# Performance work log

Hardware: AMD Instinct MI355X
Metric: run time of the kernel (lower is better)

Reference implementation:

```python
import jax, jax.numpy as jnp
import numpy as np
from jax import lax

DN = ('NCHW', 'OIHW', 'NCHW')


def setup_inputs() -> dict:
    key = jax.random.key(0)
    ks = jax.random.split(key, 7)
    B, IC, OC, H, W = 8, 64, 64, 128, 128
    return {
        'x': jax.random.normal(ks[0], (B, IC, H, W), jnp.float32),
        'w3': jax.random.normal(ks[1], (OC, IC, 3, 3), jnp.float32) * 0.05,
        'b3': jax.random.normal(ks[2], (OC,), jnp.float32) * 0.05,
        'w5': jax.random.normal(ks[3], (OC, IC, 5, 5), jnp.float32) * 0.05,
        'b5': jax.random.normal(ks[4], (OC,), jnp.float32) * 0.05,
        'wr': jax.random.normal(ks[5], (OC, 10, 1, 1), jnp.float32) * 0.1,
        'br': jax.random.normal(ks[6], (OC,), jnp.float32) * 0.05,
    }


def reference(x, w3, b3, w5, b5, wr, br):
    # Two 'same' convs (k=3 pad 1, k=5 pad 2) as in layers['5']
    y3 = lax.conv_general_dilated(x, w3, (1, 1), 'SAME', dimension_numbers=DN) + b3[None, :, None, None]
    y5 = lax.conv_general_dilated(x, w5, (1, 1), 'SAME', dimension_numbers=DN) + b5[None, :, None, None]
    B, C, H, W = y3.shape
    # The nested pad/crop loop == 9 zero-padded unit shifts of y3:
    # stackedFeatures order per channel: [y5, shift(sh=0,sw=0..2), shift(sh=1,...), ...]
    # shifted[h, w] = y3[h + 1 - sw, w + 1 - sh] with zero padding.
    P = jnp.pad(y3, ((0, 0), (0, 0), (1, 1), (1, 1)))
    shifts = [P[:, :, 2 - sw:2 - sw + H, 2 - sh:2 - sh + W]
              for sh in range(3) for sw in range(3)]
    stacked = jnp.stack([y5] + shifts, axis=2)  # [B, C, 10, H, W]
    # remap: grouped 1x1 conv, groups=OC, 10 in-channels per group
    out = jnp.einsum('bcghw,cg->bchw', stacked, wr[:, :, 0, 0]) + br[None, :, None, None]
    return out
```

## Files before the change

kernel.cpp:

```cpp
#include <hip/hip_runtime.h>

typedef unsigned short u16;
typedef unsigned int u32;
typedef __attribute__((ext_vector_type(8))) short short8;
typedef __attribute__((ext_vector_type(4))) short short4v;
typedef __attribute__((ext_vector_type(4))) float floatx4;

#define HH 128
#define WW 128
#define ICN 64
#define OCN 64
#define XP 72

__device__ __forceinline__ float bf2f(u16 u) {
    u32 b = ((u32)u) << 16;
    return __builtin_bit_cast(float, b);
}
__device__ __forceinline__ u16 f2bf(float f) {
    u32 b = __builtin_bit_cast(u32, f);
    b += 0x7FFFu + ((b >> 16) & 1u);
    return (u16)(b >> 16);
}

#define W3P_BYTE 256
#define W5P_BYTE 74240
#define SCAL_BYTE 279296
#define XT_BYTE 282624
#define Y3T_BYTE 17059840
#define N_W3P 36864
#define N_W5P 102400
#define N_SCAL 832
#define PACK_N (N_W3P + N_W5P + N_SCAL)

__global__ __launch_bounds__(256) void sniff_kernel(const u16* __restrict__ xu,
                                                    int* __restrict__ flag) {
    __shared__ int cnt;
    if (threadIdx.x == 0) cnt = 0;
    __syncthreads();
    int c = 0;
    for (int k = 0; k < 8; ++k) {
        int idx = 2 * (threadIdx.x * 8 + k);
        u16 u = xu[idx];
        int e = (u >> 7) & 0xFF;
        if (e >= 140) c++;
    }
    atomicAdd(&cnt, c);
    __syncthreads();
    if (threadIdx.x == 0) *flag = (cnt >= 8) ? 1 : 0;
}

__device__ __forceinline__ float load_any(const void* p, int i, int isf32) {
    return isf32 ? ((const float*)p)[i] : bf2f(((const u16*)p)[i]);
}

__global__ __launch_bounds__(256) void prepack(
        const void* w3, const void* b3, const void* w5, const void* b5,
        const void* wr, const void* br, const int* __restrict__ flag,
        u16* __restrict__ w3p, u16* __restrict__ w5p, float* __restrict__ scal) {
    int i = blockIdx.x * 256 + threadIdx.x;
    if (i >= PACK_N) return;
    int f = *flag;
    if (i < N_W3P + N_W5P) {
        int is5 = (i >= N_W3P);
        int ii = is5 ? i - N_W3P : i;
        int j = ii & 7, lane = (ii >> 3) & 63, mt = (ii >> 9) & 3, ks = ii >> 11;
        int oc = mt * 16 + (lane & 15);
        int k = ks * 32 + ((lane >> 4) & 3) * 8 + j;
        int tap = k >> 6, ic = k & 63;
        float v;
        if (is5) v = load_any(w5, (oc * 64 + ic) * 25 + tap, f);
        else     v = load_any(w3, (oc * 64 + ic) * 9 + tap, f);
        u16 o = f2bf(v);
        if (is5) w5p[ii] = o; else w3p[ii] = o;
    } else {
        int i2 = i - N_W3P - N_W5P;
        float v;
        if (i2 < 64)       v = load_any(b3, i2, f);
        else if (i2 < 128) v = load_any(b5, i2 - 64, f);
        else if (i2 < 768) v = load_any(wr, i2 - 128, f);
        else               v = load_any(br, i2 - 768, f);
        scal[i2] = v;
    }
}

__global__ __launch_bounds__(256) void transpose_x(
        const void* __restrict__ x, const int* __restrict__ flag,
        u16* __restrict__ xt) {
    __shared__ u16 tbuf[32 * XP];
    const int b = blockIdx.z, h = blockIdx.y, w0 = blockIdx.x * 32;
    const int t = threadIdx.x;
    const int f = *flag;
    if (f) {
        const int w2 = t & 15, ic = t >> 4;
#pragma unroll
        for (int p = 0; p < 4; ++p) {
            int icc = ic + p * 16;
            const float* src = (const float*)x +
                (((size_t)(b * 64 + icc) * 128 + h) * 128 + w0 + 2 * w2);
            float2 v = *(const float2*)src;
            tbuf[(2 * w2) * XP + icc]     = f2bf(v.x);
            tbuf[(2 * w2 + 1) * XP + icc] = f2bf(v.y);
        }
    } else {
        const int w4 = t & 7, ic = t >> 3;
#pragma unroll
        for (int p = 0; p < 2; ++p) {
            int icc = ic + p * 32;
            const u16* src = (const u16*)x +
                (((size_t)(b * 64 + icc) * 128 + h) * 128 + w0 + 4 * w4);
            short4v v = *(const short4v*)src;
#pragma unroll
            for (int e = 0; e < 4; ++e)
                tbuf[(4 * w4 + e) * XP + icc] = (u16)v[e];
        }
    }
    __syncthreads();
    const int w = t >> 3, q = t & 7;
    short8 v = *(const short8*)&tbuf[w * XP + q * 8];
    *(short8*)(xt + ((size_t)((b * 128 + h) * 128) + w0 + w) * 64 + q * 8) = v;
}

__device__ __forceinline__ void stage_tile(
        const u16* __restrict__ src, u16* __restrict__ dst,
        int b, int h0, int w0, int halo, int cols, int npx, int iters, int tid) {
    const int q8 = tid & 7, p0 = tid >> 3;
    for (int it = 0; it < iters; ++it) {
        int px = p0 + it * 32;
        if (px < npx) {
            int r = px / cols, c = px - r * cols;
            int gh = h0 + r - halo, gw = w0 + c - halo;
            short8 v = {0, 0, 0, 0, 0, 0, 0, 0};
            if ((unsigned)gh < (unsigned)HH && (unsigned)gw < (unsigned)WW)
                v = *(const short8*)(src +
                        ((size_t)((b * 128 + gh) * 128 + gw)) * 64 + q8 * 8);
            *(short8*)&dst[px * XP + q8 * 8] = v;
        }
    }
}

#define LOAD_A(dst, wp, ks)                                                    \
    {                                                                          \
        const u16* _ap = (wp) + (size_t)(ks) * 2048 + lane * 8;                \
        _Pragma("unroll") for (int _s = 0; _s < 2; ++_s)                       \
            _Pragma("unroll") for (int _mt = 0; _mt < 4; ++_mt)                \
                dst[_s][_mt] = *(const short8*)(_ap + _s * 2048 + _mt * 512);  \
    }

#define DO_TAP(afr, kh, kw, COLS)                                              \
    {                                                                          \
        short8 bb[2][4];                                                       \
        int rbase = (wv4 + (kh)) * (COLS) + cb + (kw);                         \
        _Pragma("unroll") for (int nt = 0; nt < 4; ++nt)                       \
            _Pragma("unroll") for (int s = 0; s < 2; ++s)                      \
                bb[s][nt] = *(const short8*)&xs[(rbase + nt * (COLS)) * XP +   \
                                                s * 32 + q * 8];               \
        _Pragma("unroll") for (int s = 0; s < 2; ++s)                          \
            _Pragma("unroll") for (int nt = 0; nt < 4; ++nt)                   \
                _Pragma("unroll") for (int mt = 0; mt < 4; ++mt)               \
                    acc[mt][nt] = __builtin_amdgcn_mfma_f32_16x16x32_bf16(     \
                        afr[s][mt], bb[s][nt], acc[mt][nt], 0, 0, 0);          \
    }

__global__ __launch_bounds__(256, 2) void conv3_mfma(
        const u16* __restrict__ xt, const u16* __restrict__ w3p,
        const float* __restrict__ scal, u16* __restrict__ y3t) {
    __shared__ u16 xs[324 * XP];
    const int b = blockIdx.z, h0 = blockIdx.y * 16, w0 = blockIdx.x * 16;
    const int tid = threadIdx.x;
    stage_tile(xt, xs, b, h0, w0, 1, 18, 324, 11, tid);
    __syncthreads();

    const int wv = tid >> 6, lane = tid & 63, cb = lane & 15, q = lane >> 4;
    const int wv4 = wv * 4;
    floatx4 acc[4][4];
#pragma unroll
    for (int mt = 0; mt < 4; ++mt)
#pragma unroll
        for (int nt = 0; nt < 4; ++nt)
            acc[mt][nt] = (floatx4){0.f, 0.f, 0.f, 0.f};

    short8 aA[2][4], aB[2][4];
    LOAD_A(aA, w3p, 0);
    int khA = 0, kwA = 0, khB = 0, kwB = 1;
#pragma unroll 1
    for (int t2 = 0; t2 < 4; ++t2) {
        LOAD_A(aB, w3p, (2 * t2 + 1) * 2);
        DO_TAP(aA, khA, kwA, 18);
        LOAD_A(aA, w3p, (2 * t2 + 2) * 2);
        DO_TAP(aB, khB, kwB, 18);
        kwA += 2; if (kwA >= 3) { kwA -= 3; khA++; }
        kwB += 2; if (kwB >= 3) { kwB -= 3; khB++; }
    }
    DO_TAP(aA, 2, 2, 18);

    __syncthreads();
    u16* yb = xs;
    const float* b3f = scal;
#pragma unroll
    for (int mt = 0; mt < 4; ++mt)
#pragma unroll
        for (int nt = 0; nt < 4; ++nt) {
            int px = (wv4 + nt) * 16 + cb;
#pragma unroll
            for (int p2 = 0; p2 < 2; ++p2) {
                int oc0 = mt * 16 + q * 4 + 2 * p2;
                u32 lo = f2bf(acc[mt][nt][2 * p2]     + b3f[oc0]);
                u32 hi = f2bf(acc[mt][nt][2 * p2 + 1] + b3f[oc0 + 1]);
                *(u32*)&yb[px * XP + oc0] = lo | (hi << 16);
            }
        }
    __syncthreads();
    for (int it = 0; it < 8; ++it) {
        int u = tid + 256 * it;
        int px = u >> 3, q8 = u & 7;
        short8 v = *(const short8*)&yb[px * XP + q8 * 8];
        int gh = h0 + (px >> 4), gw = w0 + (px & 15);
        *(short8*)(y3t + ((size_t)((b * 128 + gh) * 128 + gw)) * 64 + q8 * 8) = v;
    }
}

__global__ __launch_bounds__(256, 2) void conv5_mfma(
        const u16* __restrict__ xt, const u16* __restrict__ w5p,
        const float* __restrict__ scal, const int* __restrict__ flag,
        const u16* __restrict__ y3t, void* __restrict__ out) {
    __shared__ u16 xs[400 * XP];
    const int b = blockIdx.z, h0 = blockIdx.y * 16, w0 = blockIdx.x * 16;
    const int tid = threadIdx.x;
    const int f = *flag;
    stage_tile(xt, xs, b, h0, w0, 2, 20, 400, 13, tid);
    __syncthreads();

    const int wv = tid >> 6, lane = tid & 63, cb = lane & 15, q = lane >> 4;
    const int wv4 = wv * 4;
    floatx4 acc[4][4];
#pragma unroll
    for (int mt = 0; mt < 4; ++mt)
#pragma unroll
        for (int nt = 0; nt < 4; ++nt)
            acc[mt][nt] = (floatx4){0.f, 0.f, 0.f, 0.f};

    short8 aA[2][4], aB[2][4];
    LOAD_A(aA, w5p, 0);
    int khA = 0, kwA = 0, khB = 0, kwB = 1;
#pragma unroll 1
    for (int t2 = 0; t2 < 12; ++t2) {
        LOAD_A(aB, w5p, (2 * t2 + 1) * 2);
        DO_TAP(aA, khA, kwA, 20);
        LOAD_A(aA, w5p, (2 * t2 + 2) * 2);
        DO_TAP(aB, khB, kwB, 20);
        kwA += 2; if (kwA >= 5) { kwA -= 5; khA++; }
        kwB += 2; if (kwB >= 5) { kwB -= 5; khB++; }
    }
    DO_TAP(aA, 4, 4, 20);

    __syncthreads();
    u16* ys = xs;
    stage_tile(y3t, ys, b, h0, w0, 1, 18, 324, 11, tid);
    __syncthreads();

    const float* b5f = scal + 64;
    const float* wrf = scal + 128;
    const float* brf = scal + 768;
#pragma unroll
    for (int mt = 0; mt < 4; ++mt)
#pragma unroll
        for (int nt = 0; nt < 4; ++nt) {
            int row = wv4 + nt;
            int gh = h0 + row;
#pragma unroll
            for (int reg = 0; reg < 4; ++reg) {
                int oc = mt * 16 + q * 4 + reg;
                float y5 = acc[mt][nt][reg] + b5f[oc];
                float s = wrf[oc * 10] * y5 + brf[oc];
#pragma unroll
                for (int sh = 0; sh < 3; ++sh)
#pragma unroll
                    for (int sw = 0; sw < 3; ++sw) {
                        float yv = bf2f(ys[((row + 2 - sw) * 18 + (cb + 2 - sh)) * XP + oc]);
                        s = fmaf(wrf[oc * 10 + 1 + sh * 3 + sw], yv, s);
                    }
                size_t oidx = ((size_t)(b * OCN + oc) * HH + gh) * WW + w0 + cb;
                if (f) ((float*)out)[oidx] = s;
                else   ((u16*)out)[oidx]   = f2bf(s);
            }
        }
}

extern "C" void kernel_launch(void* const* d_in, const int* in_sizes, int n_in,
                              void* d_out, int out_size, void* d_ws, size_t ws_size,
                              hipStream_t stream) {
    const void* x  = d_in[0];
    const void* w3 = d_in[1];
    const void* b3 = d_in[2];
    const void* w5 = d_in[3];
    const void* b5 = d_in[4];
    const void* wr = d_in[5];
    const void* br = d_in[6];

    int*   flag = (int*)d_ws;
    u16*   w3p  = (u16*)((char*)d_ws + W3P_BYTE);
    u16*   w5p  = (u16*)((char*)d_ws + W5P_BYTE);
    float* scal = (float*)((char*)d_ws + SCAL_BYTE);
    u16*   xt   = (u16*)((char*)d_ws + XT_BYTE);
    u16*   y3t  = (u16*)((char*)d_ws + Y3T_BYTE);

    sniff_kernel<<<1, 256, 0, stream>>>((const u16*)x, flag);
    prepack<<<(PACK_N + 255) / 256, 256, 0, stream>>>(w3, b3, w5, b5, wr, br, flag,
                                                      w3p, w5p, scal);
    transpose_x<<<dim3(4, 128, 8), 256, 0, stream>>>(x, flag, xt);

    dim3 grid(WW / 16, HH / 16, 8);
    conv3_mfma<<<grid, 256, 0, stream>>>(xt, w3p, scal, y3t);
    conv5_mfma<<<grid, 256, 0, stream>>>(xt, w5p, scal, flag, y3t, d_out);
}
```

Measured before the change: 152.6 us.

## Fold remap weights into conv5 and do shift-sum via diagonal MFMA

Scales the 5x5 weights and bias by the remap's first weight and folds br into the bias. The 3x3 shifted-sum epilogue becomes a diagonal-weight MFMA pass over the staged y3 tile, replacing the scalar per-element LDS reads and FMAs. Output tiles shrink to 8x16 pixels with halved accumulators, and launch bounds rise to four blocks per CU for more occupancy. In exchange the diagonal pass spends MFMA work on mostly-zero weights, and smaller tiles mean more halo reloading.

```diff
diff --git a/kernel.cpp b/kernel.cpp
--- a/kernel.cpp
+++ b/kernel.cpp
@@ -8,8 +8,6 @@
 
 #define HH 128
 #define WW 128
-#define ICN 64
-#define OCN 64
 #define XP 72
 
 __device__ __forceinline__ float bf2f(u16 u) {
@@ -23,14 +21,16 @@
 }
 
 #define W3P_BYTE 256
-#define W5P_BYTE 74240
-#define SCAL_BYTE 279296
-#define XT_BYTE 282624
-#define Y3T_BYTE 17059840
+#define W5P_BYTE 73984
+#define WDW_BYTE 278784
+#define SCAL_BYTE 352512
+#define XT_BYTE 353024
+#define Y3T_BYTE 17130240
 #define N_W3P 36864
 #define N_W5P 102400
-#define N_SCAL 832
-#define PACK_N (N_W3P + N_W5P + N_SCAL)
+#define N_WDW 36864
+#define N_SCAL 128
+#define PACK_N (N_W3P + N_W5P + N_WDW + N_SCAL)
 
 __global__ __launch_bounds__(256) void sniff_kernel(const u16* __restrict__ xu,
                                                     int* __restrict__ flag) {
@@ -56,29 +56,35 @@
 __global__ __launch_bounds__(256) void prepack(
         const void* w3, const void* b3, const void* w5, const void* b5,
         const void* wr, const void* br, const int* __restrict__ flag,
-        u16* __restrict__ w3p, u16* __restrict__ w5p, float* __restrict__ scal) {
+        u16* __restrict__ w3p, u16* __restrict__ w5p, u16* __restrict__ wdw,
+        float* __restrict__ scal) {
     int i = blockIdx.x * 256 + threadIdx.x;
     if (i >= PACK_N) return;
     int f = *flag;
-    if (i < N_W3P + N_W5P) {
-        int is5 = (i >= N_W3P);
-        int ii = is5 ? i - N_W3P : i;
+    if (i < N_W3P + N_W5P + N_WDW) {
+        int which = (i < N_W3P) ? 0 : (i < N_W3P + N_W5P ? 1 : 2);
+        int ii = (which == 0) ? i : (which == 1 ? i - N_W3P : i - N_W3P - N_W5P);
         int j = ii & 7, lane = (ii >> 3) & 63, mt = (ii >> 9) & 3, ks = ii >> 11;
         int oc = mt * 16 + (lane & 15);
         int k = ks * 32 + ((lane >> 4) & 3) * 8 + j;
         int tap = k >> 6, ic = k & 63;
         float v;
-        if (is5) v = load_any(w5, (oc * 64 + ic) * 25 + tap, f);
-        else     v = load_any(w3, (oc * 64 + ic) * 9 + tap, f);
+        if (which == 0)      v = load_any(w3, (oc * 64 + ic) * 9 + tap, f);
+        else if (which == 1) v = load_any(wr, oc * 10, f) *
+                                 load_any(w5, (oc * 64 + ic) * 25 + tap, f);
+        else                 v = (ic == oc) ? load_any(wr, oc * 10 + 1 + tap, f) : 0.f;
         u16 o = f2bf(v);
-        if (is5) w5p[ii] = o; else w3p[ii] = o;
+        if (which == 0)      w3p[ii] = o;
+        else if (which == 1) w5p[ii] = o;
+        else                 wdw[ii] = o;
     } else {
-        int i2 = i - N_W3P - N_W5P;
+        int i2 = i - N_W3P - N_W5P - N_WDW;
         float v;
-        if (i2 < 64)       v = load_any(b3, i2, f);
-        else if (i2 < 128) v = load_any(b5, i2 - 64, f);
-        else if (i2 < 768) v = load_any(wr, i2 - 128, f);
-        else               v = load_any(br, i2 - 768, f);
+        if (i2 < 64) v = load_any(b3, i2, f);
+        else {
+            int c = i2 - 64;
+            v = load_any(wr, c * 10, f) * load_any(b5, c, f) + load_any(br, c, f);
+        }
         scal[i2] = v;
     }
 }
@@ -138,60 +144,60 @@
     }
 }
 
-#define LOAD_A(dst, wp, ks)                                                    \
+#define LOAD_A4(dst, wp, ks)                                                   \
     {                                                                          \
         const u16* _ap = (wp) + (size_t)(ks) * 2048 + lane * 8;                \
-        _Pragma("unroll") for (int _s = 0; _s < 2; ++_s)                       \
-            _Pragma("unroll") for (int _mt = 0; _mt < 4; ++_mt)                \
-                dst[_s][_mt] = *(const short8*)(_ap + _s * 2048 + _mt * 512);  \
-    }
-
-#define DO_TAP(afr, kh, kw, COLS)                                              \
+        dst[0] = *(const short8*)(_ap);                                        \
+        dst[1] = *(const short8*)(_ap + 512);                                  \
+        dst[2] = *(const short8*)(_ap + 1024);                                 \
+        dst[3] = *(const short8*)(_ap + 1536);                                 \
+    }
+
+#define TAP2(afr, kh, kw, s, COLS)                                             \
     {                                                                          \
-        short8 bb[2][4];                                                       \
-        int rbase = (wv4 + (kh)) * (COLS) + cb + (kw);                         \
-        _Pragma("unroll") for (int nt = 0; nt < 4; ++nt)                       \
-            _Pragma("unroll") for (int s = 0; s < 2; ++s)                      \
-                bb[s][nt] = *(const short8*)&xs[(rbase + nt * (COLS)) * XP +   \
-                                                s * 32 + q * 8];               \
-        _Pragma("unroll") for (int s = 0; s < 2; ++s)                          \
-            _Pragma("unroll") for (int nt = 0; nt < 4; ++nt)                   \
-                _Pragma("unroll") for (int mt = 0; mt < 4; ++mt)               \
-                    acc[mt][nt] = __builtin_amdgcn_mfma_f32_16x16x32_bf16(     \
-                        afr[s][mt], bb[s][nt], acc[mt][nt], 0, 0, 0);          \
-    }
-
-__global__ __launch_bounds__(256, 2) void conv3_mfma(
+        const u16* _bp = &xs[((wv2 + (kh)) * (COLS) + cb + (kw)) * XP +        \
+                             (s) * 32 + q * 8];                                \
+        short8 _b0 = *(const short8*)_bp;                                      \
+        short8 _b1 = *(const short8*)(_bp + (COLS) * XP);                      \
+        acc[0][0] = __builtin_amdgcn_mfma_f32_16x16x32_bf16(afr[0], _b0, acc[0][0], 0, 0, 0); \
+        acc[1][0] = __builtin_amdgcn_mfma_f32_16x16x32_bf16(afr[1], _b0, acc[1][0], 0, 0, 0); \
+        acc[2][0] = __builtin_amdgcn_mfma_f32_16x16x32_bf16(afr[2], _b0, acc[2][0], 0, 0, 0); \
+        acc[3][0] = __builtin_amdgcn_mfma_f32_16x16x32_bf16(afr[3], _b0, acc[3][0], 0, 0, 0); \
+        acc[0][1] = __builtin_amdgcn_mfma_f32_16x16x32_bf16(afr[0], _b1, acc[0][1], 0, 0, 0); \
+        acc[1][1] = __builtin_amdgcn_mfma_f32_16x16x32_bf16(afr[1], _b1, acc[1][1], 0, 0, 0); \
+        acc[2][1] = __builtin_amdgcn_mfma_f32_16x16x32_bf16(afr[2], _b1, acc[2][1], 0, 0, 0); \
+        acc[3][1] = __builtin_amdgcn_mfma_f32_16x16x32_bf16(afr[3], _b1, acc[3][1], 0, 0, 0); \
+    }
+
+__global__ __launch_bounds__(256, 4) void conv3_mfma(
         const u16* __restrict__ xt, const u16* __restrict__ w3p,
         const float* __restrict__ scal, u16* __restrict__ y3t) {
-    __shared__ u16 xs[324 * XP];
-    const int b = blockIdx.z, h0 = blockIdx.y * 16, w0 = blockIdx.x * 16;
+    __shared__ u16 xs[180 * XP];
+    const int b = blockIdx.z, h0 = blockIdx.y * 8, w0 = blockIdx.x * 16;
     const int tid = threadIdx.x;
-    stage_tile(xt, xs, b, h0, w0, 1, 18, 324, 11, tid);
+    stage_tile(xt, xs, b, h0, w0, 1, 18, 180, 6, tid);
     __syncthreads();
 
     const int wv = tid >> 6, lane = tid & 63, cb = lane & 15, q = lane >> 4;
-    const int wv4 = wv * 4;
-    floatx4 acc[4][4];
-#pragma unroll
-    for (int mt = 0; mt < 4; ++mt)
-#pragma unroll
-        for (int nt = 0; nt < 4; ++nt)
-            acc[mt][nt] = (floatx4){0.f, 0.f, 0.f, 0.f};
-
-    short8 aA[2][4], aB[2][4];
-    LOAD_A(aA, w3p, 0);
-    int khA = 0, kwA = 0, khB = 0, kwB = 1;
+    const int wv2 = wv * 2;
+    floatx4 acc[4][2];
+#pragma unroll
+    for (int mt = 0; mt < 4; ++mt) {
+        acc[mt][0] = (floatx4){0.f, 0.f, 0.f, 0.f};
+        acc[mt][1] = (floatx4){0.f, 0.f, 0.f, 0.f};
+    }
+
+    short8 aA[4], aB[4];
+    LOAD_A4(aA, w3p, 0);
 #pragma unroll 1
-    for (int t2 = 0; t2 < 4; ++t2) {
-        LOAD_A(aB, w3p, (2 * t2 + 1) * 2);
-        DO_TAP(aA, khA, kwA, 18);
-        LOAD_A(aA, w3p, (2 * t2 + 2) * 2);
-        DO_TAP(aB, khB, kwB, 18);
-        kwA += 2; if (kwA >= 3) { kwA -= 3; khA++; }
-        kwB += 2; if (kwB >= 3) { kwB -= 3; khB++; }
-    }
-    DO_TAP(aA, 2, 2, 18);
+    for (int kk = 0; kk < 18; kk += 2) {
+        const int tap = kk >> 1;
+        const int kh = tap / 3, kw = tap - kh * 3;
+        LOAD_A4(aB, w3p, kk + 1);
+        TAP2(aA, kh, kw, 0, 18);
+        if (kk + 2 < 18) LOAD_A4(aA, w3p, kk + 2);
+        TAP2(aB, kh, kw, 1, 18);
+    }
 
     __syncthreads();
     u16* yb = xs;
@@ -199,8 +205,8 @@
 #pragma unroll
     for (int mt = 0; mt < 4; ++mt)
 #pragma unroll
-        for (int nt = 0; nt < 4; ++nt) {
-            int px = (wv4 + nt) * 16 + cb;
+        for (int nt = 0; nt < 2; ++nt) {
+            int px = (wv2 + nt) * 16 + cb;
 #pragma unroll
             for (int p2 = 0; p2 < 2; ++p2) {
                 int oc0 = mt * 16 + q * 4 + 2 * p2;
@@ -210,7 +216,8 @@
             }
         }
     __syncthreads();
-    for (int it = 0; it < 8; ++it) {
+#pragma unroll
+    for (int it = 0; it < 4; ++it) {
         int u = tid + 256 * it;
         int px = u >> 3, q8 = u & 7;
         short8 v = *(const short8*)&yb[px * XP + q8 * 8];
@@ -219,67 +226,66 @@
     }
 }
 
-__global__ __launch_bounds__(256, 2) void conv5_mfma(
+__global__ __launch_bounds__(256, 4) void conv5_mfma(
         const u16* __restrict__ xt, const u16* __restrict__ w5p,
-        const float* __restrict__ scal, const int* __restrict__ flag,
-        const u16* __restrict__ y3t, void* __restrict__ out) {
-    __shared__ u16 xs[400 * XP];
-    const int b = blockIdx.z, h0 = blockIdx.y * 16, w0 = blockIdx.x * 16;
+        const u16* __restrict__ wdw, const float* __restrict__ scal,
+        const int* __restrict__ flag, const u16* __restrict__ y3t,
+        void* __restrict__ out) {
+    __shared__ u16 xs[240 * XP];
+    const int b = blockIdx.z, h0 = blockIdx.y * 8, w0 = blockIdx.x * 16;
     const int tid = threadIdx.x;
     const int f = *flag;
-    stage_tile(xt, xs, b, h0, w0, 2, 20, 400, 13, tid);
+    stage_tile(xt, xs, b, h0, w0, 2, 20, 240, 8, tid);
     __syncthreads();
 
     const int wv = tid >> 6, lane = tid & 63, cb = lane & 15, q = lane >> 4;
-    const int wv4 = wv * 4;
-    floatx4 acc[4][4];
+    const int wv2 = wv * 2;
+    floatx4 acc[4][2];
+#pragma unroll
+    for (int mt = 0; mt < 4; ++mt) {
+        acc[mt][0] = (floatx4){0.f, 0.f, 0.f, 0.f};
+        acc[mt][1] = (floatx4){0.f, 0.f, 0.f, 0.f};
+    }
+
+    short8 aA[4], aB[4];
+    LOAD_A4(aA, w5p, 0);
+#pragma unroll 1
+    for (int kk = 0; kk < 50; kk += 2) {
+        const int tap = kk >> 1;
+        const int kh = tap / 5, kw = tap - kh * 5;
+        LOAD_A4(aB, w5p, kk + 1);
+        TAP2(aA, kh, kw, 0, 20);
+        if (kk + 2 < 50) LOAD_A4(aA, w5p, kk + 2);
+        TAP2(aB, kh, kw, 1, 20);
+    }
+
+    __syncthreads();
+    stage_tile(y3t, xs, b, h0, w0, 1, 18, 180, 6, tid);
+    __syncthreads();
+
+    LOAD_A4(aA, wdw, 0);
+#pragma unroll 1
+    for (int kk = 0; kk < 18; kk += 2) {
+        const int g = kk >> 1;
+        const int sh = g / 3, sw = g - sh * 3;
+        const int kh = 2 - sw, kw = 2 - sh;
+        LOAD_A4(aB, wdw, kk + 1);
+        TAP2(aA, kh, kw, 0, 18);
+        if (kk + 2 < 18) LOAD_A4(aA, wdw, kk + 2);
+        TAP2(aB, kh, kw, 1, 18);
+    }
+
+    const float* bias5 = scal + 64;
 #pragma unroll
     for (int mt = 0; mt < 4; ++mt)
 #pragma unroll
-        for (int nt = 0; nt < 4; ++nt)
-            acc[mt][nt] = (floatx4){0.f, 0.f, 0.f, 0.f};
-
-    short8 aA[2][4], aB[2][4];
-    LOAD_A(aA, w5p, 0);
-    int khA = 0, kwA = 0, khB = 0, kwB = 1;
-#pragma unroll 1
-    for (int t2 = 0; t2 < 12; ++t2) {
-        LOAD_A(aB, w5p, (2 * t2 + 1) * 2);
-        DO_TAP(aA, khA, kwA, 20);
-        LOAD_A(aA, w5p, (2 * t2 + 2) * 2);
-        DO_TAP(aB, khB, kwB, 20);
-        kwA += 2; if (kwA >= 5) { kwA -= 5; khA++; }
-        kwB += 2; if (kwB >= 5) { kwB -= 5; khB++; }
-    }
-    DO_TAP(aA, 4, 4, 20);
-
-    __syncthreads();
-    u16* ys = xs;
-    stage_tile(y3t, ys, b, h0, w0, 1, 18, 324, 11, tid);
-    __syncthreads();
-
-    const float* b5f = scal + 64;
-    const float* wrf = scal + 128;
-    const float* brf = scal + 768;
-#pragma unroll
-    for (int mt = 0; mt < 4; ++mt)
-#pragma unroll
-        for (int nt = 0; nt < 4; ++nt) {
-            int row = wv4 + nt;
-            int gh = h0 + row;
+        for (int nt = 0; nt < 2; ++nt) {
+            int gh = h0 + wv2 + nt;
 #pragma unroll
             for (int reg = 0; reg < 4; ++reg) {
                 int oc = mt * 16 + q * 4 + reg;
-                float y5 = acc[mt][nt][reg] + b5f[oc];
-                float s = wrf[oc * 10] * y5 + brf[oc];
-#pragma unroll
-                for (int sh = 0; sh < 3; ++sh)
-#pragma unroll
-                    for (int sw = 0; sw < 3; ++sw) {
-                        float yv = bf2f(ys[((row + 2 - sw) * 18 + (cb + 2 - sh)) * XP + oc]);
-                        s = fmaf(wrf[oc * 10 + 1 + sh * 3 + sw], yv, s);
-                    }
-                size_t oidx = ((size_t)(b * OCN + oc) * HH + gh) * WW + w0 + cb;
+                float s = acc[mt][nt][reg] + bias5[oc];
+                size_t oidx = ((size_t)(b * 64 + oc) * HH + gh) * WW + w0 + cb;
                 if (f) ((float*)out)[oidx] = s;
                 else   ((u16*)out)[oidx]   = f2bf(s);
             }
@@ -300,16 +306,17 @@
     int*   flag = (int*)d_ws;
     u16*   w3p  = (u16*)((char*)d_ws + W3P_BYTE);
     u16*   w5p  = (u16*)((char*)d_ws + W5P_BYTE);
+    u16*   wdw  = (u16*)((char*)d_ws + WDW_BYTE);
     float* scal = (float*)((char*)d_ws + SCAL_BYTE);
     u16*   xt   = (u16*)((char*)d_ws + XT_BYTE);
     u16*   y3t  = (u16*)((char*)d_ws + Y3T_BYTE);
 
     sniff_kernel<<<1, 256, 0, stream>>>((const u16*)x, flag);
     prepack<<<(PACK_N + 255) / 256, 256, 0, stream>>>(w3, b3, w5, b5, wr, br, flag,
-                                                      w3p, w5p, scal);
+                                                      w3p, w5p, wdw, scal);
     transpose_x<<<dim3(4, 128, 8), 256, 0, stream>>>(x, flag, xt);
 
-    dim3 grid(WW / 16, HH / 16, 8);
+    dim3 grid(WW / 16, HH / 8, 8);
     conv3_mfma<<<grid, 256, 0, stream>>>(xt, w3p, scal, y3t);
-    conv5_mfma<<<grid, 256, 0, stream>>>(xt, w5p, scal, flag, y3t, d_out);
-}
+    conv5_mfma<<<grid, 256, 0, stream>>>(xt, w5p, wdw, scal, flag, y3t, d_out);
+}
```

Result: slower. 157.4 us (+3.1%).

## Fold shifted 3x3 conv and remap weights into single combined 5x5 conv with border fix

Applied to the files above, without the earlier changes.

Folds the 3x3 convolution, its nine shifted copies and the per-channel remap weights into one combined 5x5 weight set at prepack time, so only one MFMA convolution runs instead of two plus a y3 intermediate round trip. Zero-padding of y3 at image borders breaks the pure algebraic fold, so a small kernel computes virtual y3 values just outside the image and a fix-up kernel subtracts their contribution from border outputs. Weight tiles are now streamed into LDS with double-buffered global_load_lds, which adds a per-tap barrier. Costs are two extra small launches, a read-modify-write on border outputs, and rounding the combined weights to bf16.

```diff
diff --git a/kernel.cpp b/kernel.cpp
--- a/kernel.cpp
+++ b/kernel.cpp
@@ -8,8 +8,6 @@
 
 #define HH 128
 #define WW 128
-#define ICN 64
-#define OCN 64
 #define XP 72
 
 __device__ __forceinline__ float bf2f(u16 u) {
@@ -22,15 +20,19 @@
     return (u16)(b >> 16);
 }
 
-#define W3P_BYTE 256
-#define W5P_BYTE 74240
-#define SCAL_BYTE 279296
-#define XT_BYTE 282624
-#define Y3T_BYTE 17059840
-#define N_W3P 36864
-#define N_W5P 102400
-#define N_SCAL 832
-#define PACK_N (N_W3P + N_W5P + N_SCAL)
+typedef __attribute__((address_space(3))) u16 lds_u16;
+typedef const __attribute__((address_space(1))) u16 glob_u16;
+__device__ __forceinline__ void gl_lds16(const u16* g, u16* l) {
+    __builtin_amdgcn_global_load_lds((glob_u16*)g, (lds_u16*)l, 16, 0, 0);
+}
+
+#define W5C_BYTE 256
+#define SCAL_BYTE 205056
+#define V_BYTE 208128
+#define XT_BYTE 1273088
+#define N_W5C 102400
+#define N_SCAL 768
+#define PACK_N (N_W5C + N_SCAL)
 
 __global__ __launch_bounds__(256) void sniff_kernel(const u16* __restrict__ xu,
                                                     int* __restrict__ flag) {
@@ -56,29 +58,43 @@
 __global__ __launch_bounds__(256) void prepack(
         const void* w3, const void* b3, const void* w5, const void* b5,
         const void* wr, const void* br, const int* __restrict__ flag,
-        u16* __restrict__ w3p, u16* __restrict__ w5p, float* __restrict__ scal) {
+        u16* __restrict__ w5c, float* __restrict__ scal) {
     int i = blockIdx.x * 256 + threadIdx.x;
     if (i >= PACK_N) return;
     int f = *flag;
-    if (i < N_W3P + N_W5P) {
-        int is5 = (i >= N_W3P);
-        int ii = is5 ? i - N_W3P : i;
-        int j = ii & 7, lane = (ii >> 3) & 63, mt = (ii >> 9) & 3, ks = ii >> 11;
+    if (i < N_W5C) {
+        int j = i & 7, lane = (i >> 3) & 63, mt = (i >> 9) & 3, ks = i >> 11;
         int oc = mt * 16 + (lane & 15);
         int k = ks * 32 + ((lane >> 4) & 3) * 8 + j;
         int tap = k >> 6, ic = k & 63;
+        int kh = tap / 5, kw = tap - kh * 5;
+        int dh = kh - 2, dw = kw - 2;
+        float v = load_any(wr, oc * 10, f) * load_any(w5, (oc * 64 + ic) * 25 + tap, f);
+        for (int sw = 0; sw < 3; ++sw) {
+            int r = dh + sw;
+            if (r < 0 || r > 2) continue;
+            for (int sh = 0; sh < 3; ++sh) {
+                int c = dw + sh;
+                if (c < 0 || c > 2) continue;
+                v += load_any(wr, oc * 10 + 1 + sh * 3 + sw, f) *
+                     load_any(w3, (oc * 64 + ic) * 9 + r * 3 + c, f);
+            }
+        }
+        w5c[i] = f2bf(v);
+    } else {
+        int i2 = i - N_W5C;
         float v;
-        if (is5) v = load_any(w5, (oc * 64 + ic) * 25 + tap, f);
-        else     v = load_any(w3, (oc * 64 + ic) * 9 + tap, f);
-        u16 o = f2bf(v);
-        if (is5) w5p[ii] = o; else w3p[ii] = o;
-    } else {
-        int i2 = i - N_W3P - N_W5P;
-        float v;
-        if (i2 < 64)       v = load_any(b3, i2, f);
-        else if (i2 < 128) v = load_any(b5, i2 - 64, f);
-        else if (i2 < 768) v = load_any(wr, i2 - 128, f);
-        else               v = load_any(br, i2 - 768, f);
+        if (i2 < 64) {
+            int oc = i2;
+            float swr = 0.f;
+            for (int g = 1; g <= 9; ++g) swr += load_any(wr, oc * 10 + g, f);
+            v = load_any(wr, oc * 10, f) * load_any(b5, oc, f) +
+                swr * load_any(b3, oc, f) + load_any(br, oc, f);
+        } else if (i2 < 704) {
+            v = load_any(wr, i2 - 64, f);
+        } else {
+            v = load_any(b3, i2 - 704, f);
+        }
         scal[i2] = v;
     }
 }
@@ -120,118 +136,113 @@
     *(short8*)(xt + ((size_t)((b * 128 + h) * 128) + w0 + w) * 64 + q * 8) = v;
 }
 
-__device__ __forceinline__ void stage_tile(
-        const u16* __restrict__ src, u16* __restrict__ dst,
-        int b, int h0, int w0, int halo, int cols, int npx, int iters, int tid) {
-    const int q8 = tid & 7, p0 = tid >> 3;
-    for (int it = 0; it < iters; ++it) {
-        int px = p0 + it * 32;
-        if (px < npx) {
-            int r = px / cols, c = px - r * cols;
-            int gh = h0 + r - halo, gw = w0 + c - halo;
-            short8 v = {0, 0, 0, 0, 0, 0, 0, 0};
-            if ((unsigned)gh < (unsigned)HH && (unsigned)gw < (unsigned)WW)
-                v = *(const short8*)(src +
-                        ((size_t)((b * 128 + gh) * 128 + gw)) * 64 + q8 * 8);
-            *(short8*)&dst[px * XP + q8 * 8] = v;
-        }
-    }
-}
-
-#define LOAD_A(dst, wp, ks)                                                    \
-    {                                                                          \
-        const u16* _ap = (wp) + (size_t)(ks) * 2048 + lane * 8;                \
-        _Pragma("unroll") for (int _s = 0; _s < 2; ++_s)                       \
-            _Pragma("unroll") for (int _mt = 0; _mt < 4; ++_mt)                \
-                dst[_s][_mt] = *(const short8*)(_ap + _s * 2048 + _mt * 512);  \
-    }
-
-#define DO_TAP(afr, kh, kw, COLS)                                              \
-    {                                                                          \
-        short8 bb[2][4];                                                       \
-        int rbase = (wv4 + (kh)) * (COLS) + cb + (kw);                         \
-        _Pragma("unroll") for (int nt = 0; nt < 4; ++nt)                       \
-            _Pragma("unroll") for (int s = 0; s < 2; ++s)                      \
-                bb[s][nt] = *(const short8*)&xs[(rbase + nt * (COLS)) * XP +   \
-                                                s * 32 + q * 8];               \
-        _Pragma("unroll") for (int s = 0; s < 2; ++s)                          \
-            _Pragma("unroll") for (int nt = 0; nt < 4; ++nt)                   \
-                _Pragma("unroll") for (int mt = 0; mt < 4; ++mt)               \
-                    acc[mt][nt] = __builtin_amdgcn_mfma_f32_16x16x32_bf16(     \
-                        afr[s][mt], bb[s][nt], acc[mt][nt], 0, 0, 0);          \
-    }
-
-__global__ __launch_bounds__(256, 2) void conv3_mfma(
-        const u16* __restrict__ xt, const u16* __restrict__ w3p,
-        const float* __restrict__ scal, u16* __restrict__ y3t) {
-    __shared__ u16 xs[324 * XP];
-    const int b = blockIdx.z, h0 = blockIdx.y * 16, w0 = blockIdx.x * 16;
-    const int tid = threadIdx.x;
-    stage_tile(xt, xs, b, h0, w0, 1, 18, 324, 11, tid);
-    __syncthreads();
-
-    const int wv = tid >> 6, lane = tid & 63, cb = lane & 15, q = lane >> 4;
-    const int wv4 = wv * 4;
-    floatx4 acc[4][4];
-#pragma unroll
-    for (int mt = 0; mt < 4; ++mt)
-#pragma unroll
-        for (int nt = 0; nt < 4; ++nt)
-            acc[mt][nt] = (floatx4){0.f, 0.f, 0.f, 0.f};
-
-    short8 aA[2][4], aB[2][4];
-    LOAD_A(aA, w3p, 0);
-    int khA = 0, kwA = 0, khB = 0, kwB = 1;
-#pragma unroll 1
-    for (int t2 = 0; t2 < 4; ++t2) {
-        LOAD_A(aB, w3p, (2 * t2 + 1) * 2);
-        DO_TAP(aA, khA, kwA, 18);
-        LOAD_A(aA, w3p, (2 * t2 + 2) * 2);
-        DO_TAP(aB, khB, kwB, 18);
-        kwA += 2; if (kwA >= 3) { kwA -= 3; khA++; }
-        kwB += 2; if (kwB >= 3) { kwB -= 3; khB++; }
-    }
-    DO_TAP(aA, 2, 2, 18);
-
-    __syncthreads();
-    u16* yb = xs;
-    const float* b3f = scal;
-#pragma unroll
-    for (int mt = 0; mt < 4; ++mt)
-#pragma unroll
-        for (int nt = 0; nt < 4; ++nt) {
-            int px = (wv4 + nt) * 16 + cb;
-#pragma unroll
-            for (int p2 = 0; p2 < 2; ++p2) {
-                int oc0 = mt * 16 + q * 4 + 2 * p2;
-                u32 lo = f2bf(acc[mt][nt][2 * p2]     + b3f[oc0]);
-                u32 hi = f2bf(acc[mt][nt][2 * p2 + 1] + b3f[oc0 + 1]);
-                *(u32*)&yb[px * XP + oc0] = lo | (hi << 16);
-            }
-        }
-    __syncthreads();
-    for (int it = 0; it < 8; ++it) {
-        int u = tid + 256 * it;
-        int px = u >> 3, q8 = u & 7;
-        short8 v = *(const short8*)&yb[px * XP + q8 * 8];
-        int gh = h0 + (px >> 4), gw = w0 + (px & 15);
-        *(short8*)(y3t + ((size_t)((b * 128 + gh) * 128 + gw)) * 64 + q8 * 8) = v;
-    }
-}
-
-__global__ __launch_bounds__(256, 2) void conv5_mfma(
-        const u16* __restrict__ xt, const u16* __restrict__ w5p,
+__global__ __launch_bounds__(256) void virt_y3(
+        const void* __restrict__ x, const void* __restrict__ w3,
         const float* __restrict__ scal, const int* __restrict__ flag,
-        const u16* __restrict__ y3t, void* __restrict__ out) {
-    __shared__ u16 xs[400 * XP];
+        float* __restrict__ V) {
+    const int side = blockIdx.x, b = blockIdx.y;
+    const int t = threadIdx.x;
+    const int f = *flag;
+    const int oc = t & 63;
+    const int pidx = blockIdx.z * 4 + (t >> 6);
+    const float* b3f = scal + 704;
+    const int fixed_rc = (side == 0) ? 0 : (side == 1 ? 127 : (side == 2 ? 0 : 127));
+    const int ktap = (side == 0) ? 2 : (side == 1 ? 0 : (side == 2 ? 2 : 0));
+    for (int pos = pidx; pos < 130; pos += 16) {
+        int coord = pos - 1;
+        float acc = b3f[oc];
+        for (int ic = 0; ic < 64; ++ic) {
+            const int wbase = (oc * 64 + ic) * 9;
+#pragma unroll
+            for (int kk = 0; kk < 3; ++kk) {
+                int cc = coord + kk - 1;
+                if ((unsigned)cc >= 128u) continue;
+                float wv, xv;
+                if (side < 2) {
+                    wv = load_any(w3, wbase + ktap * 3 + kk, f);
+                    xv = load_any(x, ((b * 64 + ic) * 128 + fixed_rc) * 128 + cc, f);
+                } else {
+                    wv = load_any(w3, wbase + kk * 3 + ktap, f);
+                    xv = load_any(x, ((b * 64 + ic) * 128 + cc) * 128 + fixed_rc, f);
+                }
+                acc = fmaf(wv, xv, acc);
+            }
+        }
+        V[((size_t)(b * 4 + side) * 130 + pos) * 64 + oc] = acc;
+    }
+}
+
+__global__ __launch_bounds__(256) void apply_fix(
+        const float* __restrict__ V, const float* __restrict__ scal,
+        const int* __restrict__ flag, void* __restrict__ out) {
+    const int side = blockIdx.x, b = blockIdx.y;
+    const int f = *flag;
+    const float* wrf = scal + 64;
+    const float* Vb = V + (size_t)b * 4 * 130 * 64;
+    const float* VT = Vb;
+    const float* VB = Vb + 130 * 64;
+    const float* VL = Vb + 2 * 130 * 64;
+    const float* VR = Vb + 3 * 130 * 64;
+    const int nitems = (side < 2) ? 128 * 64 : 126 * 64;
+    for (int idx = blockIdx.z * 256 + threadIdx.x; idx < nitems; idx += 512) {
+        int oc = idx & 63;
+        int h, w;
+        if (side < 2) { w = idx >> 6; h = side ? 127 : 0; }
+        else          { h = (idx >> 6) + 1; w = (side == 2) ? 0 : 127; }
+        float s = 0.f;
+#pragma unroll
+        for (int sh = 0; sh < 3; ++sh)
+#pragma unroll
+            for (int sw = 0; sw < 3; ++sw) {
+                int qh = h + 1 - sw, qw = w + 1 - sh;
+                float v;
+                if (qh == -1)       v = VT[(qw + 1) * 64 + oc];
+                else if (qh == 128) v = VB[(qw + 1) * 64 + oc];
+                else if (qw == -1)  v = VL[(qh + 1) * 64 + oc];
+                else if (qw == 128) v = VR[(qh + 1) * 64 + oc];
+                else continue;
+                s -= wrf[oc * 10 + 1 + sh * 3 + sw] * v;
+            }
+        size_t oidx = ((size_t)(b * 64 + oc) * 128 + h) * 128 + w;
+        if (f) ((float*)out)[oidx] += s;
+        else {
+            u16* po = (u16*)out + oidx;
+            *po = f2bf(bf2f(*po) + s);
+        }
+    }
+}
+
+__global__ __launch_bounds__(256, 2) void conv_main(
+        const u16* __restrict__ xt, const u16* __restrict__ w5c,
+        const float* __restrict__ scal, const int* __restrict__ flag,
+        void* __restrict__ out) {
+    __shared__ __align__(16) u16 xs[400 * XP];
+    __shared__ __align__(16) u16 wbuf[2][2][2048];
     const int b = blockIdx.z, h0 = blockIdx.y * 16, w0 = blockIdx.x * 16;
     const int tid = threadIdx.x;
     const int f = *flag;
-    stage_tile(xt, xs, b, h0, w0, 2, 20, 400, 13, tid);
+    const int wv = tid >> 6, lane = tid & 63;
+
+    {
+        const int q8 = tid & 7, p0 = tid >> 3;
+        for (int it = 0; it < 13; ++it) {
+            int px = p0 + it * 32;
+            if (px < 400) {
+                int r = px / 20, c = px - r * 20;
+                int gh = h0 + r - 2, gw = w0 + c - 2;
+                short8 v = {0, 0, 0, 0, 0, 0, 0, 0};
+                if ((unsigned)gh < 128u && (unsigned)gw < 128u)
+                    v = *(const short8*)(xt +
+                            ((size_t)((b * 128 + gh) * 128 + gw)) * 64 + q8 * 8);
+                *(short8*)&xs[px * XP + q8 * 8] = v;
+            }
+        }
+    }
+    gl_lds16(w5c + 0 * 2048 + wv * 512 + lane * 8, &wbuf[0][0][wv * 512]);
+    gl_lds16(w5c + 1 * 2048 + wv * 512 + lane * 8, &wbuf[0][1][wv * 512]);
     __syncthreads();
 
-    const int wv = tid >> 6, lane = tid & 63, cb = lane & 15, q = lane >> 4;
-    const int wv4 = wv * 4;
+    const int cb = lane & 15, q = lane >> 4, wv4 = wv * 4;
     floatx4 acc[4][4];
 #pragma unroll
     for (int mt = 0; mt < 4; ++mt)
@@ -239,47 +250,47 @@
         for (int nt = 0; nt < 4; ++nt)
             acc[mt][nt] = (floatx4){0.f, 0.f, 0.f, 0.f};
 
-    short8 aA[2][4], aB[2][4];
-    LOAD_A(aA, w5p, 0);
-    int khA = 0, kwA = 0, khB = 0, kwB = 1;
 #pragma unroll 1
-    for (int t2 = 0; t2 < 12; ++t2) {
-        LOAD_A(aB, w5p, (2 * t2 + 1) * 2);
-        DO_TAP(aA, khA, kwA, 20);
-        LOAD_A(aA, w5p, (2 * t2 + 2) * 2);
-        DO_TAP(aB, khB, kwB, 20);
-        kwA += 2; if (kwA >= 5) { kwA -= 5; khA++; }
-        kwB += 2; if (kwB >= 5) { kwB -= 5; khB++; }
-    }
-    DO_TAP(aA, 4, 4, 20);
-
-    __syncthreads();
-    u16* ys = xs;
-    stage_tile(y3t, ys, b, h0, w0, 1, 18, 324, 11, tid);
-    __syncthreads();
-
-    const float* b5f = scal + 64;
-    const float* wrf = scal + 128;
-    const float* brf = scal + 768;
+    for (int tap = 0; tap < 25; ++tap) {
+        const int p = tap & 1;
+        if (tap + 1 < 25) {
+            gl_lds16(w5c + (size_t)((tap + 1) * 2 + 0) * 2048 + wv * 512 + lane * 8,
+                     &wbuf[p ^ 1][0][wv * 512]);
+            gl_lds16(w5c + (size_t)((tap + 1) * 2 + 1) * 2048 + wv * 512 + lane * 8,
+                     &wbuf[p ^ 1][1][wv * 512]);
+        }
+        const int kh = tap / 5, kw = tap - kh * 5;
+#pragma unroll
+        for (int s = 0; s < 2; ++s) {
+            short8 aa[4], bb[4];
+#pragma unroll
+            for (int mt = 0; mt < 4; ++mt)
+                aa[mt] = *(const short8*)&wbuf[p][s][mt * 512 + lane * 8];
+#pragma unroll
+            for (int nt = 0; nt < 4; ++nt)
+                bb[nt] = *(const short8*)&xs[((wv4 + nt + kh) * 20 + cb + kw) * XP +
+                                             s * 32 + q * 8];
+#pragma unroll
+            for (int nt = 0; nt < 4; ++nt)
+#pragma unroll
+                for (int mt = 0; mt < 4; ++mt)
+                    acc[mt][nt] = __builtin_amdgcn_mfma_f32_16x16x32_bf16(
+                        aa[mt], bb[nt], acc[mt][nt], 0, 0, 0);
+        }
+        __syncthreads();
+    }
+
+    const float* biasC = scal;
 #pragma unroll
     for (int mt = 0; mt < 4; ++mt)
 #pragma unroll
         for (int nt = 0; nt < 4; ++nt) {
-            int row = wv4 + nt;
-            int gh = h0 + row;
+            int gh = h0 + wv4 + nt;
 #pragma unroll
             for (int reg = 0; reg < 4; ++reg) {
                 int oc = mt * 16 + q * 4 + reg;
-                float y5 = acc[mt][nt][reg] + b5f[oc];
-                float s = wrf[oc * 10] * y5 + brf[oc];
-#pragma unroll
-                for (int sh = 0; sh < 3; ++sh)
-#pragma unroll
-                    for (int sw = 0; sw < 3; ++sw) {
-                        float yv = bf2f(ys[((row + 2 - sw) * 18 + (cb + 2 - sh)) * XP + oc]);
-                        s = fmaf(wrf[oc * 10 + 1 + sh * 3 + sw], yv, s);
-                    }
-                size_t oidx = ((size_t)(b * OCN + oc) * HH + gh) * WW + w0 + cb;
+                float s = acc[mt][nt][reg] + biasC[oc];
+                size_t oidx = ((size_t)(b * 64 + oc) * 128 + gh) * 128 + w0 + cb;
                 if (f) ((float*)out)[oidx] = s;
                 else   ((u16*)out)[oidx]   = f2bf(s);
             }
@@ -298,18 +309,16 @@
     const void* br = d_in[6];
 
     int*   flag = (int*)d_ws;
-    u16*   w3p  = (u16*)((char*)d_ws + W3P_BYTE);
-    u16*   w5p  = (u16*)((char*)d_ws + W5P_BYTE);
+    u16*   w5c  = (u16*)((char*)d_ws + W5C_BYTE);
     float* scal = (float*)((char*)d_ws + SCAL_BYTE);
+    float* V    = (float*)((char*)d_ws + V_BYTE);
     u16*   xt   = (u16*)((char*)d_ws + XT_BYTE);
-    u16*   y3t  = (u16*)((char*)d_ws + Y3T_BYTE);
 
     sniff_kernel<<<1, 256, 0, stream>>>((const u16*)x, flag);
     prepack<<<(PACK_N + 255) / 256, 256, 0, stream>>>(w3, b3, w5, b5, wr, br, flag,
-                                                      w3p, w5p, scal);
+                                                      w5c, scal);
     transpose_x<<<dim3(4, 128, 8), 256, 0, stream>>>(x, flag, xt);
-
-    dim3 grid(WW / 16, HH / 16, 8);
-    conv3_mfma<<<grid, 256, 0, stream>>>(xt, w3p, scal, y3t);
-    conv5_mfma<<<grid, 256, 0, stream>>>(xt, w5p, scal, flag, y3t, d_out);
-}
+    virt_y3<<<dim3(4, 8, 4), 256, 0, stream>>>(x, w3, scal, flag, V);
+    conv_main<<<dim3(8, 8, 8), 256, 0, stream>>>(xt, w5c, scal, flag, d_out);
+    apply_fix<<<dim3(4, 8, 2), 256, 0, stream>>>(V, scal, flag, d_out);
+}
```

Result: slower. 590.3 us (+286.7%).
